# Optimization experiments

Hardware: AMD Instinct MI355X
Metric: run time of the kernel (lower is better)

The kernel has to match this reference:

```python
import jax, jax.numpy as jnp
import numpy as np

LEVELS = 7
DOMAIN = 10.0
BASE_SIGMA = 0.9
HURST = 0.8
MOUNTAIN_BIAS = 0.6
COARSE_SIZE = max(2, 2 ** (LEVELS - 3))  # 16
N_POINTS = 32768


def _grid(size):
    axis = jnp.linspace(-1.0, 1.0, size)
    cx, cy = jnp.meshgrid(axis, axis, indexing='ij')
    return cx, cy


def _radial_taper(cx, cy, sharpness):
    return jnp.exp(-sharpness * (cx * cx + cy * cy))


def setup_inputs() -> dict:
    key = jax.random.key(0)
    ks = jax.random.split(key, LEVELS + 2)
    # coords uniform over [-domain, domain]
    coords = (jax.random.uniform(ks[0], (N_POINTS, 2), dtype=jnp.float32) * 2.0 - 1.0) * DOMAIN
    # scaling coeffs: N(1.1, 0.35) * (0.45 + 0.9 * taper(1.8))
    cx, cy = _grid(COARSE_SIZE)
    scaling = 1.1 + 0.35 * jax.random.normal(ks[1], (COARSE_SIZE, COARSE_SIZE), dtype=jnp.float32)
    scaling = scaling * (0.45 + 0.9 * _radial_taper(cx, cy, 1.8))
    out = {'coords': coords, 'scaling_coeffs': scaling}
    for level in range(LEVELS):
        size = 2 ** level
        amp = 2.0 ** (-HURST * level)
        c = (0.22 * MOUNTAIN_BIAS * amp
             + 0.55 * amp * jax.random.normal(ks[2 + level], (size, size), dtype=jnp.float32))
        dcx, dcy = _grid(size)
        c = c * (0.3 + 0.9 * _radial_taper(dcx, dcy, 0.9 + 0.2 * level))
        out[f'detail{level}'] = c
    return out


def _ricker_sum(xy, coeffs, cx, cy, sigma):
    sigma2 = float(sigma) ** 2 + 1e-8
    dx = xy[:, None, None, 0] - cx[None, :, :]
    dy = xy[:, None, None, 1] - cy[None, :, :]
    r2 = (dx * dx + dy * dy) / sigma2  # [N, s, s]
    basis = (2.0 - r2) * jnp.exp(-0.5 * r2)
    return jnp.einsum('bij,ij->b', basis, coeffs)


def _scaling_sum(xy, scaling_coeffs):
    cx, cy = _grid(COARSE_SIZE)
    sigma2 = (BASE_SIGMA * 1.6) ** 2
    dx = xy[:, None, None, 0] - cx[None, :, :]
    dy = xy[:, None, None, 1] - cy[None, :, :]
    r2 = (dx * dx + dy * dy) / sigma2
    return jnp.einsum('bij,ij->b', jnp.exp(-0.5 * r2), scaling_coeffs)


def reference(coords, scaling_coeffs, detail0, detail1, detail2, detail3, detail4, detail5, detail6):
    details = [detail0, detail1, detail2, detail3, detail4, detail5, detail6]
    xy = coords / DOMAIN
    out = _scaling_sum(xy, scaling_coeffs)
    for level, coeff in enumerate(details):
        sigma = BASE_SIGMA / (2 ** level)
        cx, cy = _grid(2 ** level)
        out = out + _ricker_sum(xy, coeff, cx, cy, sigma)
    return jax.nn.softplus(out)
```

## Files before the change

### kernel.cpp

```cpp
#include <hip/hip_runtime.h>
#include <math.h>

#define NPOINTS 32768
#define LOG2E 1.4426950408889634


template<int SZ>
__device__ __forceinline__ float ricker_full(float x, float y,
                                             const float* __restrict__ c) {
  const double s2d = (0.9 / SZ) * (0.9 / SZ) + 1e-8;
  const float K  = (float)(-0.5 * LOG2E / s2d);
  const float BS = (float)(-1.0 / s2d);
  const float sp = (SZ > 1) ? 2.0f / (float)(SZ - 1) : 0.0f;
  float acc = 0.0f;
  for (int i = 0; i < SZ; ++i) {
    float cx = (SZ == 1) ? -1.0f : fmaf((float)i, sp, -1.0f);
    float dx = x - cx;
    float dx2 = dx * dx;
#pragma unroll
    for (int j = 0; j < SZ; ++j) {
      float cy = (SZ == 1) ? -1.0f : fmaf((float)j, sp, -1.0f);
      float dy = y - cy;
      float r2 = fmaf(dy, dy, dx2);
      float t = fmaf(BS, r2, 2.0f);
      acc = fmaf(c[i * SZ + j] * t, __builtin_amdgcn_exp2f(K * r2), acc);
    }
  }
  return acc;
}

template<int SZ>
__device__ __forceinline__ float ricker_win(float x, float y,
                                            const float* __restrict__ c) {
  const double s2d = (0.9 / SZ) * (0.9 / SZ) + 1e-8;
  const float K  = (float)(-0.5 * LOG2E / s2d);
  const float BS = (float)(-1.0 / s2d);
  const float sp = 2.0f / (float)(SZ - 1);
  const float inv_sp = (float)(SZ - 1) * 0.5f;
  int i0 = (int)floorf(fmaf(x + 1.0f, inv_sp, -3.5f));
  int j0 = (int)floorf(fmaf(y + 1.0f, inv_sp, -3.5f));
  i0 = min(max(i0, 0), SZ - 8);
  j0 = min(max(j0, 0), SZ - 8);
  float cx0 = fmaf((float)i0, sp, -1.0f);
  float cy0 = fmaf((float)j0, sp, -1.0f);
  float acc = 0.0f;
  for (int i = 0; i < 8; ++i) {
    float dx = x - fmaf((float)i, sp, cx0);
    float dx2 = dx * dx;
    const float* row = c + (i0 + i) * SZ + j0;
#pragma unroll
    for (int j = 0; j < 8; ++j) {
      float dy = y - fmaf((float)j, sp, cy0);
      float r2 = fmaf(dy, dy, dx2);
      float t = fmaf(BS, r2, 2.0f);
      acc = fmaf(row[j] * t, __builtin_amdgcn_exp2f(K * r2), acc);
    }
  }
  return acc;
}

__global__ __launch_bounds__(512) void wavelet_fused(
    const float2* __restrict__ coords,
    const float* __restrict__ scaling,
    const float* __restrict__ d0, const float* __restrict__ d1,
    const float* __restrict__ d2, const float* __restrict__ d3,
    const float* __restrict__ d4, const float* __restrict__ d5,
    const float* __restrict__ d6,
    float* __restrict__ out) {
  __shared__ float red[8][64];
  int lane = threadIdx.x & 63;
  int slice = __builtin_amdgcn_readfirstlane(threadIdx.x >> 6);
  int p = blockIdx.x * 64 + lane;
  float2 c2 = coords[p];
  float x = c2.x * 0.1f;
  float y = c2.y * 0.1f;
  float acc = 0.0f;

  if (slice < 4) {
    const float KS = (float)(-0.5 * LOG2E / 2.0736);
    const float SPS = 2.0f / 15.0f;
    int base = slice * 64;
    for (int t = 0; t < 64; ++t) {
      int cell = base + t;
      int i = cell >> 4, j = cell & 15;
      float c = scaling[cell];
      float dx = x - fmaf((float)i, SPS, -1.0f);
      float dy = y - fmaf((float)j, SPS, -1.0f);
      float r2 = fmaf(dy, dy, dx * dx);
      acc = fmaf(c, __builtin_amdgcn_exp2f(KS * r2), acc);
    }
  } else if (slice == 4) {
    acc += ricker_full<1>(x, y, d0);
    acc += ricker_full<2>(x, y, d1);
    acc += ricker_full<4>(x, y, d2);
    acc += ricker_full<8>(x, y, d3);
  } else if (slice == 5) {
    acc = ricker_win<16>(x, y, d4);
  } else if (slice == 6) {
    acc = ricker_win<32>(x, y, d5);
  } else {
    acc = ricker_win<64>(x, y, d6);
  }

  red[slice][lane] = acc;
  __syncthreads();

  if (threadIdx.x < 64) {
    float s = 0.0f;
#pragma unroll
    for (int t = 0; t < 8; ++t) s += red[t][threadIdx.x];
    out[p] = fmaxf(s, 0.0f) + log1pf(__expf(-fabsf(s)));
  }
}

extern "C" void kernel_launch(void* const* d_in, const int* in_sizes, int n_in,
                              void* d_out, int out_size, void* d_ws, size_t ws_size,
                              hipStream_t stream) {
  const float2* coords = (const float2*)d_in[0];
  const float* scaling = (const float*)d_in[1];
  const float* d0 = (const float*)d_in[2];
  const float* d1 = (const float*)d_in[3];
  const float* d2 = (const float*)d_in[4];
  const float* d3 = (const float*)d_in[5];
  const float* d4 = (const float*)d_in[6];
  const float* d5 = (const float*)d_in[7];
  const float* d6 = (const float*)d_in[8];

  wavelet_fused<<<NPOINTS / 64, 512, 0, stream>>>(
      coords, scaling, d0, d1, d2, d3, d4, d5, d6, (float*)d_out);
}
```

Before: 10.77 us.

## Separate Gaussian exponentials per axis and rebalance work across wave slices

Rewrites each basis sum using exp(-(dx²+dy²)) = exp(-dx²)·exp(-dy²), so exponentials are computed per row and per column instead of per cell. The work split across the eight wave slices is rebalanced: the scaling sum goes from four slices to two, and level 3 and level 6 are each split across two slices. The windowed levels now use a 12-wide column window aligned to multiples of 4 so each row loads as float4 vectors. Risks are higher register pressure from the unrolled per-axis arrays and a window alignment that must still cover the significant support.

```diff
diff --git a/kernel.cpp b/kernel.cpp
--- a/kernel.cpp
+++ b/kernel.cpp
@@ -4,56 +4,109 @@
 #define NPOINTS 32768
 #define LOG2E 1.4426950408889634
 
+__device__ __forceinline__ float ex2(float v) { return __builtin_amdgcn_exp2f(v); }
 
-template<int SZ>
-__device__ __forceinline__ float ricker_full(float x, float y,
+
+template<int R0, int R1>
+__device__ __forceinline__ float scaling_sep(float x, float y,
                                              const float* __restrict__ c) {
+  const float KS = (float)(-0.5 * LOG2E / 2.0736);
+  const float SPS = 2.0f / 15.0f;
+  float Ey[16];
+#pragma unroll
+  for (int j = 0; j < 16; ++j) {
+    float dy = y - fmaf((float)j, SPS, -1.0f);
+    Ey[j] = ex2(KS * (dy * dy));
+  }
+  float acc = 0.0f;
+#pragma unroll
+  for (int i = R0; i < R1; ++i) {
+    float dx = x - fmaf((float)i, SPS, -1.0f);
+    float Exi = ex2(KS * (dx * dx));
+    float rd = 0.0f;
+#pragma unroll
+    for (int j = 0; j < 16; ++j) rd = fmaf(c[i * 16 + j], Ey[j], rd);
+    acc = fmaf(Exi, rd, acc);
+  }
+  return acc;
+}
+
+__device__ __forceinline__ float ricker_l0(float x, float y,
+                                           const float* __restrict__ c) {
+  const double s2d = 0.81 + 1e-8;
+  const float K = (float)(-0.5 * LOG2E / s2d);
+  const float BS = (float)(-1.0 / s2d);
+  float dx = x + 1.0f, dy = y + 1.0f;
+  float r2 = fmaf(dy, dy, dx * dx);
+  return c[0] * fmaf(BS, r2, 2.0f) * ex2(K * r2);
+}
+
+template<int SZ, int R0, int R1>
+__device__ __forceinline__ float ricker_full_sep(float x, float y,
+                                                 const float* __restrict__ c) {
   const double s2d = (0.9 / SZ) * (0.9 / SZ) + 1e-8;
-  const float K  = (float)(-0.5 * LOG2E / s2d);
+  const float K = (float)(-0.5 * LOG2E / s2d);
   const float BS = (float)(-1.0 / s2d);
-  const float sp = (SZ > 1) ? 2.0f / (float)(SZ - 1) : 0.0f;
+  const float sp = 2.0f / (float)(SZ - 1);
+  float Ey[SZ], dy2[SZ];
+#pragma unroll
+  for (int j = 0; j < SZ; ++j) {
+    float dy = y - fmaf((float)j, sp, -1.0f);
+    dy2[j] = dy * dy;
+    Ey[j] = ex2(K * dy2[j]);
+  }
   float acc = 0.0f;
-  for (int i = 0; i < SZ; ++i) {
-    float cx = (SZ == 1) ? -1.0f : fmaf((float)i, sp, -1.0f);
-    float dx = x - cx;
+#pragma unroll
+  for (int i = R0; i < R1; ++i) {
+    float dx = x - fmaf((float)i, sp, -1.0f);
     float dx2 = dx * dx;
+    float Exi = ex2(K * dx2);
+    float Ai = fmaf(BS, dx2, 2.0f);
 #pragma unroll
     for (int j = 0; j < SZ; ++j) {
-      float cy = (SZ == 1) ? -1.0f : fmaf((float)j, sp, -1.0f);
-      float dy = y - cy;
-      float r2 = fmaf(dy, dy, dx2);
-      float t = fmaf(BS, r2, 2.0f);
-      acc = fmaf(c[i * SZ + j] * t, __builtin_amdgcn_exp2f(K * r2), acc);
+      float t = fmaf(BS, dy2[j], Ai);
+      acc = fmaf(c[i * SZ + j] * t, Exi * Ey[j], acc);
     }
   }
   return acc;
 }
 
-template<int SZ>
-__device__ __forceinline__ float ricker_win(float x, float y,
-                                            const float* __restrict__ c) {
+template<int SZ, int R0, int R1>
+__device__ __forceinline__ float ricker_win_sep(float x, float y,
+                                                const float* __restrict__ c) {
   const double s2d = (0.9 / SZ) * (0.9 / SZ) + 1e-8;
-  const float K  = (float)(-0.5 * LOG2E / s2d);
+  const float K = (float)(-0.5 * LOG2E / s2d);
   const float BS = (float)(-1.0 / s2d);
   const float sp = 2.0f / (float)(SZ - 1);
   const float inv_sp = (float)(SZ - 1) * 0.5f;
-  int i0 = (int)floorf(fmaf(x + 1.0f, inv_sp, -3.5f));
-  int j0 = (int)floorf(fmaf(y + 1.0f, inv_sp, -3.5f));
-  i0 = min(max(i0, 0), SZ - 8);
-  j0 = min(max(j0, 0), SZ - 8);
+  int fi = (int)floorf((x + 1.0f) * inv_sp);
+  int fj = (int)floorf((y + 1.0f) * inv_sp);
+  int i0 = min(max(fi - 3, 0), SZ - 8);
+  int j0 = min(max((fj - 4) & ~3, 0), SZ - 12);
   float cx0 = fmaf((float)i0, sp, -1.0f);
   float cy0 = fmaf((float)j0, sp, -1.0f);
+  float Ey[12], dy2[12];
+#pragma unroll
+  for (int j = 0; j < 12; ++j) {
+    float dy = y - fmaf((float)j, sp, cy0);
+    dy2[j] = dy * dy;
+    Ey[j] = ex2(K * dy2[j]);
+  }
   float acc = 0.0f;
-  for (int i = 0; i < 8; ++i) {
+#pragma unroll
+  for (int i = R0; i < R1; ++i) {
     float dx = x - fmaf((float)i, sp, cx0);
     float dx2 = dx * dx;
-    const float* row = c + (i0 + i) * SZ + j0;
+    float Exi = ex2(K * dx2);
+    float Ai = fmaf(BS, dx2, 2.0f);
+    const float4* rp = (const float4*)(c + (i0 + i) * SZ + j0);
+    float4 ra = rp[0], rb = rp[1], rc = rp[2];
+    float rv[12] = {ra.x, ra.y, ra.z, ra.w, rb.x, rb.y, rb.z, rb.w,
+                    rc.x, rc.y, rc.z, rc.w};
 #pragma unroll
-    for (int j = 0; j < 8; ++j) {
-      float dy = y - fmaf((float)j, sp, cy0);
-      float r2 = fmaf(dy, dy, dx2);
-      float t = fmaf(BS, r2, 2.0f);
-      acc = fmaf(row[j] * t, __builtin_amdgcn_exp2f(K * r2), acc);
+    for (int j = 0; j < 12; ++j) {
+      float t = fmaf(BS, dy2[j], Ai);
+      acc = fmaf(rv[j] * t, Exi * Ey[j], acc);
     }
   }
   return acc;
@@ -76,30 +129,18 @@
   float y = c2.y * 0.1f;
   float acc = 0.0f;
 
-  if (slice < 4) {
-    const float KS = (float)(-0.5 * LOG2E / 2.0736);
-    const float SPS = 2.0f / 15.0f;
-    int base = slice * 64;
-    for (int t = 0; t < 64; ++t) {
-      int cell = base + t;
-      int i = cell >> 4, j = cell & 15;
-      float c = scaling[cell];
-      float dx = x - fmaf((float)i, SPS, -1.0f);
-      float dy = y - fmaf((float)j, SPS, -1.0f);
-      float r2 = fmaf(dy, dy, dx * dx);
-      acc = fmaf(c, __builtin_amdgcn_exp2f(KS * r2), acc);
-    }
-  } else if (slice == 4) {
-    acc += ricker_full<1>(x, y, d0);
-    acc += ricker_full<2>(x, y, d1);
-    acc += ricker_full<4>(x, y, d2);
-    acc += ricker_full<8>(x, y, d3);
-  } else if (slice == 5) {
-    acc = ricker_win<16>(x, y, d4);
-  } else if (slice == 6) {
-    acc = ricker_win<32>(x, y, d5);
-  } else {
-    acc = ricker_win<64>(x, y, d6);
+  switch (slice) {
+    case 0: acc = scaling_sep<0, 8>(x, y, scaling); break;
+    case 1: acc = scaling_sep<8, 16>(x, y, scaling); break;
+    case 2: acc = ricker_l0(x, y, d0)
+                + ricker_full_sep<2, 0, 2>(x, y, d1)
+                + ricker_full_sep<4, 0, 4>(x, y, d2)
+                + ricker_full_sep<8, 0, 4>(x, y, d3); break;
+    case 3: acc = ricker_full_sep<8, 4, 8>(x, y, d3); break;
+    case 4: acc = ricker_win_sep<16, 0, 8>(x, y, d4); break;
+    case 5: acc = ricker_win_sep<32, 0, 8>(x, y, d5); break;
+    case 6: acc = ricker_win_sep<64, 0, 4>(x, y, d6); break;
+    default: acc = ricker_win_sep<64, 4, 8>(x, y, d6); break;
   }
 
   red[slice][lane] = acc;
```

New measurement: 9.670 us. -10.2%, faster.
